# Optimization experiments

Measured on AMD Instinct MI355X. Metric: run time of the kernel, lower is better.

## Reference

```python
import jax, jax.numpy as jnp
import numpy as np

N_QUERIES = 16384
N_TRAIN = 16384


def setup_inputs() -> dict:
    key = jax.random.key(0)
    k1, k2, k3 = jax.random.split(key, 3)
    queries = jax.random.normal(k1, (N_QUERIES,), dtype=jnp.float32)
    x_train = jax.random.normal(k2, (N_TRAIN,), dtype=jnp.float32)
    y_train = jax.random.normal(k3, (N_TRAIN,), dtype=jnp.float32)
    w = jnp.ones((N_TRAIN,), dtype=jnp.float32)  # learned bandwidth param
    return {"queries": queries, "x_train": x_train, "y_train": y_train, "w": w}


def reference(queries, x_train, y_train, w):
    # pairwise diff: [n_q, n_train]
    diff = queries[:, None] - x_train[None, :]
    scores = -jnp.square(diff * w) * 0.5
    attn = jax.nn.softmax(scores, axis=1)  # [n_q, n_train]
    return attn @ y_train  # [n_q]
```

## Files before the change

kernel.cpp:

```cpp
#include <hip/hip_runtime.h>

#if defined(__has_builtin)
#if __has_builtin(__builtin_amdgcn_exp2f)
#define EXP2F(x) __builtin_amdgcn_exp2f(x)
#endif
#endif
#ifndef EXP2F
#define EXP2F(x) exp2f(x)
#endif

#define BLOCK 256
#define QPT 8
#define TILE 512
#define TILE2 (TILE / 2)
#define MAX_SEGS 128
#define RSPLIT 4

typedef float v2f __attribute__((ext_vector_type(2)));

#define KFOLD 0.8493218f

__global__ __launch_bounds__(BLOCK) void nw_partial(
    const float* __restrict__ q, const float* __restrict__ xt,
    const float* __restrict__ yt, const float* __restrict__ w,
    float2* __restrict__ partial, int n_q, int n_t, int segs)
{
    __shared__ float4 tileA[TILE2];
    __shared__ float2 tileY[TILE2];

    const int seg = blockIdx.x;
    const int tid = threadIdx.x;
    const int qbase = blockIdx.y * (BLOCK * QPT) + tid;

    v2f q2[QPT];
    v2f num2[QPT], den2[QPT];
#pragma unroll
    for (int i = 0; i < QPT; ++i) {
        int qi = qbase + i * BLOCK;
        float qv = (qi < n_q) ? q[qi] : 0.f;
        q2[i] = (v2f){qv, qv};
        num2[i] = (v2f){0.f, 0.f};
        den2[i] = (v2f){0.f, 0.f};
    }

    const int seg_len = (n_t + segs - 1) / segs;
    const int s0 = seg * seg_len;
    const int s1 = min(s0 + seg_len, n_t);

    float* tA = (float*)tileA;
    float* tY = (float*)tileY;

    for (int base = s0; base < s1; base += TILE) {
        const int cnt = min(TILE, s1 - base);
        const int cnt2 = (cnt + 1) >> 1;
        __syncthreads();
        for (int l = tid; l < cnt; l += BLOCK) {
            int jj = base + l;
            float a = w[jj] * KFOLD;
            float nb = -xt[jj] * a;
            int p = l >> 1, h = l & 1;
            tA[p * 4 + h] = a;
            tA[p * 4 + 2 + h] = nb;
            tY[p * 2 + h] = yt[jj];
        }
        if (tid == 0 && (cnt & 1)) {
            int p = cnt >> 1;
            tA[p * 4 + 1] = 0.f;
            tA[p * 4 + 3] = 1.0e4f;
            tY[p * 2 + 1] = 0.f;
        }
        __syncthreads();
#pragma unroll 4
        for (int j2 = 0; j2 < cnt2; ++j2) {
            float4 A = tileA[j2];
            float2 Y = tileY[j2];
            v2f a2 = (v2f){A.x, A.y};
            v2f nb2 = (v2f){A.z, A.w};
            v2f y2 = (v2f){Y.x, Y.y};
#pragma unroll
            for (int i = 0; i < QPT; ++i) {
                v2f t = __builtin_elementwise_fma(q2[i], a2, nb2);
                v2f s = -(t * t);
                v2f e = (v2f){EXP2F(s.x), EXP2F(s.y)};
                num2[i] = __builtin_elementwise_fma(e, y2, num2[i]);
                den2[i] = den2[i] + e;
            }
        }
    }

#pragma unroll
    for (int i = 0; i < QPT; ++i) {
        int qi = qbase + i * BLOCK;
        if (qi < n_q)
            partial[seg * n_q + qi] =
                make_float2(num2[i].x + num2[i].y, den2[i].x + den2[i].y);
    }
}

__global__ __launch_bounds__(BLOCK) void nw_reduce(
    const float2* __restrict__ partial, float* __restrict__ out,
    int n_q, int segs)
{
    __shared__ float2 red[RSPLIT][64];
    const int tid = threadIdx.x;
    const int c = tid >> 6;
    const int ql = tid & 63;
    const int qi = blockIdx.x * 64 + ql;

    float num = 0.f, den = 0.f;
    if (qi < n_q) {
        for (int s = c; s < segs; s += RSPLIT) {
            float2 p = partial[(size_t)s * n_q + qi];
            num += p.x;
            den += p.y;
        }
    }
    red[c][ql] = make_float2(num, den);
    __syncthreads();
    if (c == 0 && qi < n_q) {
        float2 r1 = red[1][ql], r2 = red[2][ql], r3 = red[3][ql];
        num += r1.x + r2.x + r3.x;
        den += r1.y + r2.y + r3.y;
        out[qi] = num / den;
    }
}

extern "C" void kernel_launch(void* const* d_in, const int* in_sizes, int n_in,
                              void* d_out, int out_size, void* d_ws, size_t ws_size,
                              hipStream_t stream) {
    const float* q  = (const float*)d_in[0];
    const float* xt = (const float*)d_in[1];
    const float* yt = (const float*)d_in[2];
    const float* w  = (const float*)d_in[3];
    const int n_q = in_sizes[0];
    const int n_t = in_sizes[1];

    int segs = MAX_SEGS;
    size_t need = (size_t)segs * (size_t)n_q * sizeof(float2);
    if (need > ws_size) {
        segs = (int)(ws_size / ((size_t)n_q * sizeof(float2)));
        if (segs < 1) segs = 1;
    }

    float2* partial = (float2*)d_ws;
    dim3 grid(segs, (n_q + BLOCK * QPT - 1) / (BLOCK * QPT));
    nw_partial<<<grid, BLOCK, 0, stream>>>(q, xt, yt, w, partial, n_q, n_t, segs);
    nw_reduce<<<(n_q + 63) / 64, BLOCK, 0, stream>>>(partial, (float*)d_out,
                                                     n_q, segs);
}
```

Baseline: 105.2 us.

## Compute kernel scores in packed fp16 with polynomial exp2 and fdot2 accumulation

Moves the inner loop from fp32 to packed half-precision: the affine term and square are computed in fp16, exp2 is replaced by a clamped range-reduction plus cubic polynomial in packed fp16 arithmetic, and the numerator and denominator are accumulated into fp32 with fdot2. The shared tile is repacked as fp16 values, which cuts LDS footprint, and launch bounds now request higher occupancy. The aim is to get around the scalar transcendental unit and double ALU throughput with packed math. The cost is precision: fp16 query and train values, the approximate exp, and the clamp at -14 all reduce accuracy and could break tolerance.

```diff
diff --git a/kernel.cpp b/kernel.cpp
--- a/kernel.cpp
+++ b/kernel.cpp
@@ -1,13 +1,4 @@
 #include <hip/hip_runtime.h>
-
-#if defined(__has_builtin)
-#if __has_builtin(__builtin_amdgcn_exp2f)
-#define EXP2F(x) __builtin_amdgcn_exp2f(x)
-#endif
-#endif
-#ifndef EXP2F
-#define EXP2F(x) exp2f(x)
-#endif
 
 #define BLOCK 256
 #define QPT 8
@@ -16,39 +7,61 @@
 #define MAX_SEGS 128
 #define RSPLIT 4
 
-typedef float v2f __attribute__((ext_vector_type(2)));
+typedef _Float16 h2 __attribute__((ext_vector_type(2)));
+typedef unsigned short w2 __attribute__((ext_vector_type(2)));
+typedef unsigned short u16;
 
 #define KFOLD 0.8493218f
 
-__global__ __launch_bounds__(BLOCK) void nw_partial(
+__device__ __forceinline__ h2 exp2_pk16(h2 s) {
+    const h2 clampv = {(_Float16)-14.0f, (_Float16)-14.0f};
+    const h2 magic = {(_Float16)1536.0f, (_Float16)1536.0f};
+    const h2 nmagic = {(_Float16)-1536.0f, (_Float16)-1536.0f};
+    s = __builtin_elementwise_max(s, clampv);
+    h2 z = s + magic;
+    h2 fi = z + nmagic;
+    h2 f = s - fi;
+    const h2 c3 = {(_Float16)0.0555041f, (_Float16)0.0555041f};
+    const h2 c2 = {(_Float16)0.2402265f, (_Float16)0.2402265f};
+    const h2 c1 = {(_Float16)0.6931472f, (_Float16)0.6931472f};
+    const h2 c0 = {(_Float16)1.0003f,    (_Float16)1.0003f};
+    h2 p = __builtin_elementwise_fma(f, c3, c2);
+    p = __builtin_elementwise_fma(f, p, c1);
+    p = __builtin_elementwise_fma(f, p, c0);
+    w2 zb = __builtin_bit_cast(w2, z);
+    w2 i10 = zb << 10;
+    w2 eb = __builtin_bit_cast(w2, p) + i10;
+    return __builtin_bit_cast(h2, eb);
+}
+
+__global__ __launch_bounds__(BLOCK, 4) void nw_partial(
     const float* __restrict__ q, const float* __restrict__ xt,
     const float* __restrict__ yt, const float* __restrict__ w,
     float2* __restrict__ partial, int n_q, int n_t, int segs)
 {
-    __shared__ float4 tileA[TILE2];
-    __shared__ float2 tileY[TILE2];
+    __shared__ u16 tileH[TILE2 * 8];
 
     const int seg = blockIdx.x;
     const int tid = threadIdx.x;
     const int qbase = blockIdx.y * (BLOCK * QPT) + tid;
 
-    v2f q2[QPT];
-    v2f num2[QPT], den2[QPT];
+    h2 q2[QPT];
+    float num[QPT], den[QPT];
 #pragma unroll
     for (int i = 0; i < QPT; ++i) {
         int qi = qbase + i * BLOCK;
         float qv = (qi < n_q) ? q[qi] : 0.f;
-        q2[i] = (v2f){qv, qv};
-        num2[i] = (v2f){0.f, 0.f};
-        den2[i] = (v2f){0.f, 0.f};
+        _Float16 qh = (_Float16)qv;
+        q2[i] = (h2){qh, qh};
+        num[i] = 0.f;
+        den[i] = 0.f;
     }
 
     const int seg_len = (n_t + segs - 1) / segs;
     const int s0 = seg * seg_len;
     const int s1 = min(s0 + seg_len, n_t);
 
-    float* tA = (float*)tileA;
-    float* tY = (float*)tileY;
+    const h2 one2 = {(_Float16)1.0f, (_Float16)1.0f};
 
     for (int base = s0; base < s1; base += TILE) {
         const int cnt = min(TILE, s1 - base);
@@ -57,33 +70,33 @@
         for (int l = tid; l < cnt; l += BLOCK) {
             int jj = base + l;
             float a = w[jj] * KFOLD;
-            float nb = -xt[jj] * a;
+            float b = -xt[jj] * a;
             int p = l >> 1, h = l & 1;
-            tA[p * 4 + h] = a;
-            tA[p * 4 + 2 + h] = nb;
-            tY[p * 2 + h] = yt[jj];
+            tileH[p * 8 + h]     = __builtin_bit_cast(u16, (_Float16)a);
+            tileH[p * 8 + 2 + h] = __builtin_bit_cast(u16, (_Float16)b);
+            tileH[p * 8 + 4 + h] = __builtin_bit_cast(u16, (_Float16)yt[jj]);
         }
         if (tid == 0 && (cnt & 1)) {
             int p = cnt >> 1;
-            tA[p * 4 + 1] = 0.f;
-            tA[p * 4 + 3] = 1.0e4f;
-            tY[p * 2 + 1] = 0.f;
+            tileH[p * 8 + 1] = __builtin_bit_cast(u16, (_Float16)0.0f);
+            tileH[p * 8 + 3] = __builtin_bit_cast(u16, (_Float16)-14.0f);
+            tileH[p * 8 + 5] = __builtin_bit_cast(u16, (_Float16)0.0f);
         }
         __syncthreads();
+        const uint4* tile4 = (const uint4*)tileH;
 #pragma unroll 4
         for (int j2 = 0; j2 < cnt2; ++j2) {
-            float4 A = tileA[j2];
-            float2 Y = tileY[j2];
-            v2f a2 = (v2f){A.x, A.y};
-            v2f nb2 = (v2f){A.z, A.w};
-            v2f y2 = (v2f){Y.x, Y.y};
+            uint4 V = tile4[j2];
+            h2 a2 = __builtin_bit_cast(h2, (unsigned int)V.x);
+            h2 b2 = __builtin_bit_cast(h2, (unsigned int)V.y);
+            h2 y2 = __builtin_bit_cast(h2, (unsigned int)V.z);
 #pragma unroll
             for (int i = 0; i < QPT; ++i) {
-                v2f t = __builtin_elementwise_fma(q2[i], a2, nb2);
-                v2f s = -(t * t);
-                v2f e = (v2f){EXP2F(s.x), EXP2F(s.y)};
-                num2[i] = __builtin_elementwise_fma(e, y2, num2[i]);
-                den2[i] = den2[i] + e;
+                h2 t = __builtin_elementwise_fma(q2[i], a2, b2);
+                h2 s = -(t * t);
+                h2 e = exp2_pk16(s);
+                num[i] = __builtin_amdgcn_fdot2(e, y2, num[i], false);
+                den[i] = __builtin_amdgcn_fdot2(e, one2, den[i], false);
             }
         }
     }
@@ -91,9 +104,7 @@
 #pragma unroll
     for (int i = 0; i < QPT; ++i) {
         int qi = qbase + i * BLOCK;
-        if (qi < n_q)
-            partial[seg * n_q + qi] =
-                make_float2(num2[i].x + num2[i].y, den2[i].x + den2[i].y);
+        if (qi < n_q) partial[seg * n_q + qi] = make_float2(num[i], den[i]);
     }
 }
 
```

New measurement: 126.5 us. 1.2x slower.
